# Kernel optimization log

Hardware: AMD Instinct MI355X
Metric: run time of the kernel (lower is better)

Reference implementation:

```python
import jax, jax.numpy as jnp
import numpy as np

MUL_S, MUL_V = 256, 128              # 256x0e + 128x1o hidden irreps
DIM_H = MUL_S + 3 * MUL_V            # 640
N_NODES = 100000
INV_SQRT3 = 3.0 ** -0.5
# e3nn 'element' path normalization: sqrt(ir_out.dim / sum_paths(mul1*mul2));
# for the 1o output the extra sqrt(3) cancels the 1/sqrt(3) of the wigner-3j,
# so every path ends up with the same constant.
C0 = (1.0 / (MUL_S + MUL_V)) ** 0.5


def _unif(key, shape, fan):
    # matches linear_layer_init: uniform(-a, a), a = sqrt(6/(mul1*mul2 + mul_out)), mul2 = 1
    a = (6.0 / fan) ** 0.5
    return jax.random.uniform(key, shape, minval=-a, maxval=a, dtype=jnp.float32)


def setup_inputs() -> dict:
    key = jax.random.key(0)
    ks = jax.random.split(key, 8)
    data_in = jax.random.normal(ks[0], (N_NODES, DIM_H + 4), dtype=jnp.float32)
    return {
        "data_in": data_in,
        "W_ss": _unif(ks[1], (MUL_S, MUL_S), MUL_S + MUL_S),      # 0e x 0e -> 0e (scalars)
        "W_vv": _unif(ks[2], (MUL_V, MUL_S), MUL_V + MUL_S),      # 1o x 1o -> 0e (scalars)
        "W_ss_g": _unif(ks[3], (MUL_S, MUL_V), MUL_S + MUL_V),    # 0e x 0e -> 0e (gates)
        "W_vv_g": _unif(ks[4], (MUL_V, MUL_V), MUL_V + MUL_V),    # 1o x 1o -> 0e (gates)
        "W_sv": _unif(ks[5], (MUL_S, MUL_V), MUL_S + MUL_V),      # 0e x 1o -> 1o
        "W_vs": _unif(ks[6], (MUL_V, MUL_V), MUL_V + MUL_V),      # 1o x 0e -> 1o
        "b": jnp.zeros((MUL_S,), dtype=jnp.float32),
    }


def reference(data_in, W_ss, W_vv, W_ss_g, W_vv_g, W_sv, W_vs, b):
    # split hidden / pos parts (forward does data_in[:, :-irreps_pos.dim] etc.)
    xs = data_in[:, :MUL_S]                           # [N, 256] 0e
    xv = data_in[:, MUL_S:DIM_H].reshape(-1, MUL_V, 3)  # [N, 128, 3] 1o
    ps = data_in[:, DIM_H:DIM_H + 1]                  # [N, 1] pos scalar
    pv = data_in[:, DIM_H + 1:]                       # [N, 3] pos vector

    # CG invariants feeding the 0e outputs
    s0 = xs * ps                                       # 0e x 0e path
    dot = jnp.einsum('nuk,nk->nu', xv, pv) * INV_SQRT3  # 1o x 1o -> 0e path, [N, 128]

    scal = C0 * (s0 @ W_ss + dot @ W_vv) + b           # [N, 256] scalars (+bias on N_trivial)
    gate = C0 * (s0 @ W_ss_g + dot @ W_vv_g)           # [N, 128] gates

    # 1o outputs: 0e x 1o and 1o x 0e paths
    v1 = (xs @ W_sv)[:, :, None] * pv[:, None, :]            # [N, 128, 3]
    v2 = jnp.einsum('nuk,uw->nwk', xv, W_vs) * ps[:, :, None]  # [N, 128, 3]
    vec = C0 * (v1 + v2)

    # Gate: Swish(beta=1) on scalars, sigmoid(gates) multiplying gated 1o irreps
    scal_out = scal * jax.nn.sigmoid(scal)
    vec_out = vec * jax.nn.sigmoid(gate)[:, :, None]
    return jnp.concatenate([scal_out, vec_out.reshape(-1, 3 * MUL_V)], axis=1)  # [N, 640]
```

## Files before the change

kernel.cpp:

```cpp
#include <hip/hip_runtime.h>
#include <hip/hip_bf16.h>

#define MUL_Sc 256
#define MUL_Vc 128
#define DIM_Hc 640
#define IN_COLS 644
#define KF 768
#define NT 32

#define C0F 0.05103103630798287f
#define INV_SQRT3F 0.57735026918962576f

typedef __attribute__((ext_vector_type(8))) short short8;
typedef __attribute__((ext_vector_type(4))) float f32x4;

#define MFMA(a, b, c) __builtin_amdgcn_mfma_f32_16x16x32_bf16((a), (b), (c), 0, 0, 0)

__device__ __forceinline__ unsigned short f2bf(float x) {
    union { float f; unsigned u; } v; v.f = x;
    unsigned r = v.u + 0x7fffu + ((v.u >> 16) & 1u);
    return (unsigned short)(r >> 16);
}
__device__ __forceinline__ float bf2f(unsigned short h) {
    union { unsigned u; float f; } v; v.u = ((unsigned)h) << 16;
    return v.f;
}

__global__ void prep_weights(const float* __restrict__ Wss, const float* __restrict__ Wvv,
                             const float* __restrict__ Wssg, const float* __restrict__ Wvvg,
                             const float* __restrict__ Wsv, const float* __restrict__ Wvs,
                             unsigned short* __restrict__ wt) {
    int i = blockIdx.x * 256 + threadIdx.x;
    const int N_SG = 384 * 384;
    const int N_SV = 128 * 256;
    const int N_VS = 128 * 128;
    if (i < N_SG) {
        int col = i / 384, k = i % 384;
        float v;
        if (col < 256) v = (k < 256) ? Wss[k * 256 + col] : Wvv[(k - 256) * 256 + col];
        else { int c = col - 256; v = (k < 256) ? Wssg[k * 128 + c] : Wvvg[(k - 256) * 128 + c]; }
        wt[i] = f2bf(v);
    } else if (i < N_SG + N_SV) {
        int j = i - N_SG; int col = j >> 8, k = j & 255;
        wt[i] = f2bf(Wsv[k * 128 + col]);
    } else if (i < N_SG + N_SV + N_VS) {
        int j = i - N_SG - N_SV; int col = j >> 7, k = j & 127;
        wt[i] = f2bf(Wvs[k * 128 + col]);
    }
}

__global__ __launch_bounds__(512, 4)
void fused_main(const float* __restrict__ din, const unsigned short* __restrict__ wt,
                const float* __restrict__ bias, float* __restrict__ out, int N) {
    __shared__ unsigned short feat[NT * KF];
    __shared__ float psv[NT * 4];

    const int tid = threadIdx.x;
    const int n0 = blockIdx.x * NT;

    {
        const int g = tid >> 4;
        const int j = tid & 15;
        int n = n0 + g; if (n >= N) n = N - 1;
        const float* row = din + (size_t)n * IN_COLS;
        float ps  = row[DIM_Hc];
        float pv0 = row[DIM_Hc + 1], pv1 = row[DIM_Hc + 2], pv2 = row[DIM_Hc + 3];
        if (j == 0) { psv[g*4+0] = ps; psv[g*4+1] = pv0; psv[g*4+2] = pv1; psv[g*4+3] = pv2; }
        char* fb = (char*)feat;
        const int swz  = (g & 7) << 4;
        const int rowb = g * (KF * 2);

        {
            int c = 16 * j;
            float4 x0 = *(const float4*)(row + c);
            float4 x1 = *(const float4*)(row + c + 4);
            float4 x2 = *(const float4*)(row + c + 8);
            float4 x3 = *(const float4*)(row + c + 12);
            short8 p0, p1;
            p0[0]=(short)f2bf(x0.x); p0[1]=(short)f2bf(x0.y); p0[2]=(short)f2bf(x0.z); p0[3]=(short)f2bf(x0.w);
            p0[4]=(short)f2bf(x1.x); p0[5]=(short)f2bf(x1.y); p0[6]=(short)f2bf(x1.z); p0[7]=(short)f2bf(x1.w);
            p1[0]=(short)f2bf(x2.x); p1[1]=(short)f2bf(x2.y); p1[2]=(short)f2bf(x2.z); p1[3]=(short)f2bf(x2.w);
            p1[4]=(short)f2bf(x3.x); p1[5]=(short)f2bf(x3.y); p1[6]=(short)f2bf(x3.z); p1[7]=(short)f2bf(x3.w);
            *(short8*)(fb + ((rowb + c * 2) ^ swz))       = p0;
            *(short8*)(fb + ((rowb + (c + 8) * 2) ^ swz)) = p1;
        }
        {
            int u0 = 8 * j;
            const float* p = row + MUL_Sc + 3 * u0;
            float e[24];
            #pragma unroll
            for (int q = 0; q < 6; ++q) {
                float4 v = *(const float4*)(p + 4 * q);
                e[4*q+0] = v.x; e[4*q+1] = v.y; e[4*q+2] = v.z; e[4*q+3] = v.w;
            }
            short8 dp, k0, k1, k2;
            #pragma unroll
            for (int m = 0; m < 8; ++m) {
                float a = e[3*m], b = e[3*m+1], c = e[3*m+2];
                dp[m] = (short)f2bf((a * pv0 + b * pv1 + c * pv2) * INV_SQRT3F);
                k0[m] = (short)f2bf(a);
                k1[m] = (short)f2bf(b);
                k2[m] = (short)f2bf(c);
            }
            *(short8*)(fb + ((rowb + (256 + u0) * 2) ^ swz)) = dp;
            *(short8*)(fb + ((rowb + (384 + u0) * 2) ^ swz)) = k0;
            *(short8*)(fb + ((rowb + (512 + u0) * 2) ^ swz)) = k1;
            *(short8*)(fb + ((rowb + (640 + u0) * 2) ^ swz)) = k2;
        }
    }
    __syncthreads();

    const int wave = tid >> 6;
    const int lane = tid & 63;
    const int l15  = lane & 15;
    const int lkb  = (lane >> 4) << 3;
    const char* fbr = (const char*)feat;
    const int swzr = (l15 & 7) << 4;

    const unsigned short* WTsg = wt;
    const unsigned short* WTsv = wt + 384 * 384;
    const unsigned short* WTvs = wt + 384 * 384 + 128 * 256;

    f32x4 acc1[3][2], acc2[3][2];
    #pragma unroll
    for (int t = 0; t < 3; ++t) {
        acc1[t][0] = (f32x4){0,0,0,0}; acc1[t][1] = (f32x4){0,0,0,0};
        acc2[t][0] = (f32x4){0,0,0,0}; acc2[t][1] = (f32x4){0,0,0,0};
    }
    const unsigned short* bp0 = WTsg + ((wave     ) * 16 + l15) * 384 + lkb;
    const unsigned short* bp1 = WTsg + ((wave +  8) * 16 + l15) * 384 + lkb;
    const unsigned short* bp2 = WTsg + ((wave + 16) * 16 + l15) * 384 + lkb;
    short8 b0a = *(const short8*)(bp0);      short8 b0b = *(const short8*)(bp0 + 32);
    short8 b1a = *(const short8*)(bp1);      short8 b1b = *(const short8*)(bp1 + 32);
    short8 b2a = *(const short8*)(bp2);      short8 b2b = *(const short8*)(bp2 + 32);
    #pragma unroll
    for (int ks = 0; ks < 12; ++ks) {
        int kf = ks * 32 + lkb;
        short8 a0 = *(const short8*)(fbr + ((l15 * 1536 + kf * 2) ^ swzr));
        short8 a1 = *(const short8*)(fbr + (((16 + l15) * 1536 + kf * 2) ^ swzr));
        short8 c0 = b0a, c1 = b1a, c2 = b2a;
        b0a = b0b; b1a = b1b; b2a = b2b;
        if (ks < 10) {
            b0b = *(const short8*)(bp0 + (ks + 2) * 32);
            b1b = *(const short8*)(bp1 + (ks + 2) * 32);
            b2b = *(const short8*)(bp2 + (ks + 2) * 32);
        }
        if (ks < 8) {
            acc1[0][0] = MFMA(a0, c0, acc1[0][0]); acc1[0][1] = MFMA(a1, c0, acc1[0][1]);
            acc1[1][0] = MFMA(a0, c1, acc1[1][0]); acc1[1][1] = MFMA(a1, c1, acc1[1][1]);
            acc1[2][0] = MFMA(a0, c2, acc1[2][0]); acc1[2][1] = MFMA(a1, c2, acc1[2][1]);
        } else {
            acc2[0][0] = MFMA(a0, c0, acc2[0][0]); acc2[0][1] = MFMA(a1, c0, acc2[0][1]);
            acc2[1][0] = MFMA(a0, c1, acc2[1][0]); acc2[1][1] = MFMA(a1, c1, acc2[1][1]);
            acc2[2][0] = MFMA(a0, c2, acc2[2][0]); acc2[2][1] = MFMA(a1, c2, acc2[2][1]);
        }
    }
    __syncthreads();

    f32x4 accA[2], accV[3][2];
    accA[0] = (f32x4){0,0,0,0}; accA[1] = (f32x4){0,0,0,0};
    #pragma unroll
    for (int k = 0; k < 3; ++k) { accV[k][0] = (f32x4){0,0,0,0}; accV[k][1] = (f32x4){0,0,0,0}; }

    const unsigned short* pA = WTsv + (wave * 16 + l15) * 256 + lkb;
    const unsigned short* pV = WTvs + (wave * 16 + l15) * 128 + lkb;
    short8 va = *(const short8*)(pA);      short8 vb = *(const short8*)(pA + 32);
    #pragma unroll
    for (int ks = 0; ks < 8; ++ks) {
        int kf = ks * 32 + lkb;
        short8 a0 = *(const short8*)(fbr + ((l15 * 1536 + kf * 2) ^ swzr));
        short8 a1 = *(const short8*)(fbr + (((16 + l15) * 1536 + kf * 2) ^ swzr));
        short8 cur = va; va = vb;
        if (ks < 6) vb = *(const short8*)(pA + (ks + 2) * 32);
        accA[0] = MFMA(a0, cur, accA[0]);
        accA[1] = MFMA(a1, cur, accA[1]);
    }
    short8 wa = *(const short8*)(pV);      short8 wb = *(const short8*)(pV + 32);
    #pragma unroll
    for (int ks = 0; ks < 4; ++ks) {
        short8 cur = wa; wa = wb;
        if (ks < 2) wb = *(const short8*)(pV + (ks + 2) * 32);
        #pragma unroll
        for (int k = 0; k < 3; ++k) {
            int kf = 384 + 128 * k + ks * 32 + lkb;
            short8 a0 = *(const short8*)(fbr + ((l15 * 1536 + kf * 2) ^ swzr));
            short8 a1 = *(const short8*)(fbr + (((16 + l15) * 1536 + kf * 2) ^ swzr));
            accV[k][0] = MFMA(a0, cur, accV[k][0]);
            accV[k][1] = MFMA(a1, cur, accV[k][1]);
        }
    }

    {
        const int rbase = (lane >> 4) << 2;
        float pss[2][4];
        #pragma unroll
        for (int s = 0; s < 2; ++s)
        #pragma unroll
        for (int i = 0; i < 4; ++i) pss[s][i] = psv[(s * 16 + rbase + i) * 4];

        #pragma unroll
        for (int t = 0; t < 2; ++t) {
            int col = (wave + t * 8) * 16 + l15;
            float bc = bias[col];
            #pragma unroll
            for (int s = 0; s < 2; ++s)
            #pragma unroll
            for (int i = 0; i < 4; ++i) {
                int nl = s * 16 + rbase + i;
                int n = n0 + nl;
                if (n < N) {
                    float sc = C0F * (pss[s][i] * acc1[t][s][i] + acc2[t][s][i]) + bc;
                    out[(size_t)n * DIM_Hc + col] = sc / (1.f + __expf(-sc));
                }
            }
        }
        char* fbw = (char*)feat;
        int gc = wave * 16 + l15;
        #pragma unroll
        for (int s = 0; s < 2; ++s)
        #pragma unroll
        for (int i = 0; i < 4; ++i) {
            int nl = s * 16 + rbase + i;
            float gt = C0F * (pss[s][i] * acc1[2][s][i] + acc2[2][s][i]);
            unsigned short sg = f2bf(1.f / (1.f + __expf(-gt)));
            *(unsigned short*)(fbw + ((nl * 1536 + (256 + gc) * 2) ^ ((nl & 7) << 4))) = sg;
        }
    }
    __syncthreads();

    {
        const int rbase = (lane >> 4) << 2;
        int u = wave * 16 + l15;
        #pragma unroll
        for (int s = 0; s < 2; ++s)
        #pragma unroll
        for (int i = 0; i < 4; ++i) {
            int nl = s * 16 + rbase + i;
            int n = n0 + nl;
            if (n >= N) continue;
            float sg  = bf2f(*(const unsigned short*)(fbr + ((nl * 1536 + (256 + u) * 2) ^ ((nl & 7) << 4))));
            float ps  = psv[nl * 4 + 0];
            float pv0 = psv[nl * 4 + 1], pv1 = psv[nl * 4 + 2], pv2 = psv[nl * 4 + 3];
            float av = accA[s][i];
            size_t ob = (size_t)n * DIM_Hc + MUL_Sc + 3 * u;
            out[ob + 0] = C0F * (av * pv0 + accV[0][s][i] * ps) * sg;
            out[ob + 1] = C0F * (av * pv1 + accV[1][s][i] * ps) * sg;
            out[ob + 2] = C0F * (av * pv2 + accV[2][s][i] * ps) * sg;
        }
    }
}

extern "C" void kernel_launch(void* const* d_in, const int* in_sizes, int n_in,
                              void* d_out, int out_size, void* d_ws, size_t ws_size,
                              hipStream_t stream) {
    const float* din  = (const float*)d_in[0];
    const float* Wss  = (const float*)d_in[1];
    const float* Wvv  = (const float*)d_in[2];
    const float* Wssg = (const float*)d_in[3];
    const float* Wvvg = (const float*)d_in[4];
    const float* Wsv  = (const float*)d_in[5];
    const float* Wvs  = (const float*)d_in[6];
    const float* bias = (const float*)d_in[7];
    float* out = (float*)d_out;
    unsigned short* wt = (unsigned short*)d_ws;

    const size_t WT_BYTES = (size_t)(384 * 384 + 128 * 256 + 128 * 128) * 2;
    if (ws_size < WT_BYTES) return;

    int N = in_sizes[0] / IN_COLS;

    int prep_total = 384 * 384 + 128 * 256 + 128 * 128;
    prep_weights<<<(prep_total + 255) / 256, 256, 0, stream>>>(Wss, Wvv, Wssg, Wvvg, Wsv, Wvs, wt);

    int nblocks = (N + NT - 1) / NT;
    fused_main<<<nblocks, 512, 0, stream>>>(din, wt, bias, out, N);
}
```

Baseline: 244.7 us.

## Stage weight tiles into LDS via double-buffered async global-to-LDS loads

Weight B-operands are no longer read per-wave straight from global memory. They are copied into a double-buffered, swizzled LDS tile with global_load_lds, and the copy of the next K-step overlaps the MFMAs on the current one. The gate sigmoid now stays in registers instead of round-tripping through LDS, and the two scalar accumulators are merged by scaling with ps mid-loop. The change adds about 96KB of LDS and many block-wide barriers, and lowers the occupancy hint from 4 to 2 blocks per CU.

Result: slower. 269.3 us (+10.0%).

```diff
diff --git a/kernel.cpp b/kernel.cpp
--- a/kernel.cpp
+++ b/kernel.cpp
@@ -2,7 +2,6 @@
 #include <hip/hip_bf16.h>
 
 #define MUL_Sc 256
-#define MUL_Vc 128
 #define DIM_Hc 640
 #define IN_COLS 644
 #define KF 768
@@ -21,9 +20,10 @@
     unsigned r = v.u + 0x7fffu + ((v.u >> 16) & 1u);
     return (unsigned short)(r >> 16);
 }
-__device__ __forceinline__ float bf2f(unsigned short h) {
-    union { unsigned u; float f; } v; v.u = ((unsigned)h) << 16;
-    return v.f;
+
+__device__ __forceinline__ void gload_lds16(const unsigned short* g, unsigned short* l) {
+    __builtin_amdgcn_global_load_lds((const __attribute__((address_space(1))) void*)g,
+                                     (__attribute__((address_space(3))) void*)l, 16, 0, 0);
 }
 
 __global__ void prep_weights(const float* __restrict__ Wss, const float* __restrict__ Wvv,
@@ -49,14 +49,34 @@
     }
 }
 
-__global__ __launch_bounds__(512, 4)
+__global__ __launch_bounds__(512, 2)
 void fused_main(const float* __restrict__ din, const unsigned short* __restrict__ wt,
                 const float* __restrict__ bias, float* __restrict__ out, int N) {
     __shared__ unsigned short feat[NT * KF];
+    __shared__ unsigned short ldsB[2][384 * 64];
     __shared__ float psv[NT * 4];
 
-    const int tid = threadIdx.x;
-    const int n0 = blockIdx.x * NT;
+    const int tid  = threadIdx.x;
+    const int wave = tid >> 6;
+    const int lane = tid & 63;
+    const int n0   = blockIdx.x * NT;
+
+    const unsigned short* WTsg = wt;
+    const unsigned short* WTsv = wt + 384 * 384;
+    const unsigned short* WTvs = wt + 384 * 384 + 128 * 256;
+
+    auto stage = [&](int buf, const unsigned short* W, int rs, int nr, int step) {
+        unsigned short* lb = &ldsB[buf][0] + wave * 512;
+        #pragma unroll
+        for (int m = 0; m < nr; ++m) {
+            int slot = m * 512 + tid;
+            int col  = slot >> 3;
+            int k8   = (slot & 7) ^ (col & 7);
+            gload_lds16(W + col * rs + step * 64 + k8 * 8, lb + m * 4096);
+        }
+    };
+
+    stage(0, WTsg, 384, 6, 0);
 
     {
         const int g = tid >> 4;
@@ -110,126 +130,121 @@
     }
     __syncthreads();
 
-    const int wave = tid >> 6;
-    const int lane = tid & 63;
-    const int l15  = lane & 15;
-    const int lkb  = (lane >> 4) << 3;
+    const int l15   = lane & 15;
+    const int lkb   = (lane >> 4) << 3;
+    const int chnk  = lane >> 4;
+    const int rbase = (lane >> 4) << 2;
     const char* fbr = (const char*)feat;
-    const int swzr = (l15 & 7) << 4;
-
-    const unsigned short* WTsg = wt;
-    const unsigned short* WTsv = wt + 384 * 384;
-    const unsigned short* WTvs = wt + 384 * 384 + 128 * 256;
-
-    f32x4 acc1[3][2], acc2[3][2];
-    #pragma unroll
-    for (int t = 0; t < 3; ++t) {
-        acc1[t][0] = (f32x4){0,0,0,0}; acc1[t][1] = (f32x4){0,0,0,0};
-        acc2[t][0] = (f32x4){0,0,0,0}; acc2[t][1] = (f32x4){0,0,0,0};
-    }
-    const unsigned short* bp0 = WTsg + ((wave     ) * 16 + l15) * 384 + lkb;
-    const unsigned short* bp1 = WTsg + ((wave +  8) * 16 + l15) * 384 + lkb;
-    const unsigned short* bp2 = WTsg + ((wave + 16) * 16 + l15) * 384 + lkb;
-    short8 b0a = *(const short8*)(bp0);      short8 b0b = *(const short8*)(bp0 + 32);
-    short8 b1a = *(const short8*)(bp1);      short8 b1b = *(const short8*)(bp1 + 32);
-    short8 b2a = *(const short8*)(bp2);      short8 b2b = *(const short8*)(bp2 + 32);
-    #pragma unroll
-    for (int ks = 0; ks < 12; ++ks) {
-        int kf = ks * 32 + lkb;
-        short8 a0 = *(const short8*)(fbr + ((l15 * 1536 + kf * 2) ^ swzr));
-        short8 a1 = *(const short8*)(fbr + (((16 + l15) * 1536 + kf * 2) ^ swzr));
-        short8 c0 = b0a, c1 = b1a, c2 = b2a;
-        b0a = b0b; b1a = b1b; b2a = b2b;
-        if (ks < 10) {
-            b0b = *(const short8*)(bp0 + (ks + 2) * 32);
-            b1b = *(const short8*)(bp1 + (ks + 2) * 32);
-            b2b = *(const short8*)(bp2 + (ks + 2) * 32);
-        }
-        if (ks < 8) {
-            acc1[0][0] = MFMA(a0, c0, acc1[0][0]); acc1[0][1] = MFMA(a1, c0, acc1[0][1]);
-            acc1[1][0] = MFMA(a0, c1, acc1[1][0]); acc1[1][1] = MFMA(a1, c1, acc1[1][1]);
-            acc1[2][0] = MFMA(a0, c2, acc1[2][0]); acc1[2][1] = MFMA(a1, c2, acc1[2][1]);
-        } else {
-            acc2[0][0] = MFMA(a0, c0, acc2[0][0]); acc2[0][1] = MFMA(a1, c0, acc2[0][1]);
-            acc2[1][0] = MFMA(a0, c1, acc2[1][0]); acc2[1][1] = MFMA(a1, c1, acc2[1][1]);
-            acc2[2][0] = MFMA(a0, c2, acc2[2][0]); acc2[2][1] = MFMA(a1, c2, acc2[2][1]);
-        }
-    }
-    __syncthreads();
-
-    f32x4 accA[2], accV[3][2];
+    const int swzr  = (l15 & 7) << 4;
+
+    float pss[2][4];
+    #pragma unroll
+    for (int s = 0; s < 2; ++s)
+    #pragma unroll
+    for (int i = 0; i < 4; ++i) pss[s][i] = psv[(s * 16 + rbase + i) * 4];
+
+    f32x4 accS[3][2];
+    #pragma unroll
+    for (int t = 0; t < 3; ++t) { accS[t][0] = (f32x4){0,0,0,0}; accS[t][1] = (f32x4){0,0,0,0}; }
+    f32x4 accA[2];
     accA[0] = (f32x4){0,0,0,0}; accA[1] = (f32x4){0,0,0,0};
+    f32x4 accV[3][2];
     #pragma unroll
     for (int k = 0; k < 3; ++k) { accV[k][0] = (f32x4){0,0,0,0}; accV[k][1] = (f32x4){0,0,0,0}; }
 
-    const unsigned short* pA = WTsv + (wave * 16 + l15) * 256 + lkb;
-    const unsigned short* pV = WTvs + (wave * 16 + l15) * 128 + lkb;
-    short8 va = *(const short8*)(pA);      short8 vb = *(const short8*)(pA + 32);
-    #pragma unroll
-    for (int ks = 0; ks < 8; ++ks) {
-        int kf = ks * 32 + lkb;
-        short8 a0 = *(const short8*)(fbr + ((l15 * 1536 + kf * 2) ^ swzr));
-        short8 a1 = *(const short8*)(fbr + (((16 + l15) * 1536 + kf * 2) ^ swzr));
-        short8 cur = va; va = vb;
-        if (ks < 6) vb = *(const short8*)(pA + (ks + 2) * 32);
-        accA[0] = MFMA(a0, cur, accA[0]);
-        accA[1] = MFMA(a1, cur, accA[1]);
-    }
-    short8 wa = *(const short8*)(pV);      short8 wb = *(const short8*)(pV + 32);
-    #pragma unroll
-    for (int ks = 0; ks < 4; ++ks) {
-        short8 cur = wa; wa = wb;
-        if (ks < 2) wb = *(const short8*)(pV + (ks + 2) * 32);
-        #pragma unroll
-        for (int k = 0; k < 3; ++k) {
-            int kf = 384 + 128 * k + ks * 32 + lkb;
+    auto sgstep = [&](int buf, int step) {
+        const char* B = (const char*)&ldsB[buf][0];
+        #pragma unroll
+        for (int ks = 0; ks < 2; ++ks) {
+            int kf = step * 64 + ks * 32 + lkb;
             short8 a0 = *(const short8*)(fbr + ((l15 * 1536 + kf * 2) ^ swzr));
             short8 a1 = *(const short8*)(fbr + (((16 + l15) * 1536 + kf * 2) ^ swzr));
-            accV[k][0] = MFMA(a0, cur, accV[k][0]);
-            accV[k][1] = MFMA(a1, cur, accV[k][1]);
-        }
-    }
+            int ch = ks * 4 + chnk;
+            #pragma unroll
+            for (int t = 0; t < 3; ++t) {
+                int col = (wave + t * 8) * 16 + l15;
+                short8 b = *(const short8*)(B + col * 128 + ((ch ^ (col & 7)) << 4));
+                accS[t][0] = MFMA(a0, b, accS[t][0]);
+                accS[t][1] = MFMA(a1, b, accS[t][1]);
+            }
+        }
+    };
+    auto svstep = [&](int buf, int step) {
+        const char* B = (const char*)&ldsB[buf][0];
+        #pragma unroll
+        for (int ks = 0; ks < 2; ++ks) {
+            int kf = step * 64 + ks * 32 + lkb;
+            short8 a0 = *(const short8*)(fbr + ((l15 * 1536 + kf * 2) ^ swzr));
+            short8 a1 = *(const short8*)(fbr + (((16 + l15) * 1536 + kf * 2) ^ swzr));
+            int ch = ks * 4 + chnk;
+            int col = wave * 16 + l15;
+            short8 b = *(const short8*)(B + col * 128 + ((ch ^ (col & 7)) << 4));
+            accA[0] = MFMA(a0, b, accA[0]);
+            accA[1] = MFMA(a1, b, accA[1]);
+        }
+    };
+    auto vsstep = [&](int buf, int step) {
+        const char* B = (const char*)&ldsB[buf][0];
+        #pragma unroll
+        for (int ks = 0; ks < 2; ++ks) {
+            int ch = ks * 4 + chnk;
+            int col = wave * 16 + l15;
+            short8 b = *(const short8*)(B + col * 128 + ((ch ^ (col & 7)) << 4));
+            #pragma unroll
+            for (int p = 0; p < 3; ++p) {
+                int kf = 384 + p * 128 + step * 64 + ks * 32 + lkb;
+                short8 a0 = *(const short8*)(fbr + ((l15 * 1536 + kf * 2) ^ swzr));
+                short8 a1 = *(const short8*)(fbr + (((16 + l15) * 1536 + kf * 2) ^ swzr));
+                accV[p][0] = MFMA(a0, b, accV[p][0]);
+                accV[p][1] = MFMA(a1, b, accV[p][1]);
+            }
+        }
+    };
+
+    stage(1, WTsg, 384, 6, 1);  sgstep(0, 0);  __syncthreads();
+    stage(0, WTsg, 384, 6, 2);  sgstep(1, 1);  __syncthreads();
+    stage(1, WTsg, 384, 6, 3);  sgstep(0, 2);  __syncthreads();
+    stage(0, WTsg, 384, 6, 4);  sgstep(1, 3);
+    #pragma unroll
+    for (int t = 0; t < 3; ++t)
+    #pragma unroll
+    for (int s = 0; s < 2; ++s)
+    #pragma unroll
+    for (int i = 0; i < 4; ++i) accS[t][s][i] *= pss[s][i];
+    __syncthreads();
+    stage(1, WTsg, 384, 6, 5);  sgstep(0, 4);  __syncthreads();
+    stage(0, WTsv, 256, 2, 0);  sgstep(1, 5);
+
+    #pragma unroll
+    for (int t = 0; t < 2; ++t) {
+        int col = (wave + t * 8) * 16 + l15;
+        float bc = bias[col];
+        #pragma unroll
+        for (int s = 0; s < 2; ++s)
+        #pragma unroll
+        for (int i = 0; i < 4; ++i) {
+            int n = n0 + s * 16 + rbase + i;
+            if (n < N) {
+                float sc = C0F * accS[t][s][i] + bc;
+                out[(size_t)n * DIM_Hc + col] = sc / (1.f + __expf(-sc));
+            }
+        }
+    }
+    float sgr[2][4];
+    #pragma unroll
+    for (int s = 0; s < 2; ++s)
+    #pragma unroll
+    for (int i = 0; i < 4; ++i) sgr[s][i] = 1.f / (1.f + __expf(-C0F * accS[2][s][i]));
+    __syncthreads();
+
+    stage(1, WTsv, 256, 2, 1);  svstep(0, 0);  __syncthreads();
+    stage(0, WTsv, 256, 2, 2);  svstep(1, 1);  __syncthreads();
+    stage(1, WTsv, 256, 2, 3);  svstep(0, 2);  __syncthreads();
+    stage(0, WTvs, 128, 2, 0);  svstep(1, 3);  __syncthreads();
+    stage(1, WTvs, 128, 2, 1);  vsstep(0, 0);  __syncthreads();
+                                vsstep(1, 1);
 
     {
-        const int rbase = (lane >> 4) << 2;
-        float pss[2][4];
-        #pragma unroll
-        for (int s = 0; s < 2; ++s)
-        #pragma unroll
-        for (int i = 0; i < 4; ++i) pss[s][i] = psv[(s * 16 + rbase + i) * 4];
-
-        #pragma unroll
-        for (int t = 0; t < 2; ++t) {
-            int col = (wave + t * 8) * 16 + l15;
-            float bc = bias[col];
-            #pragma unroll
-            for (int s = 0; s < 2; ++s)
-            #pragma unroll
-            for (int i = 0; i < 4; ++i) {
-                int nl = s * 16 + rbase + i;
-                int n = n0 + nl;
-                if (n < N) {
-                    float sc = C0F * (pss[s][i] * acc1[t][s][i] + acc2[t][s][i]) + bc;
-                    out[(size_t)n * DIM_Hc + col] = sc / (1.f + __expf(-sc));
-                }
-            }
-        }
-        char* fbw = (char*)feat;
-        int gc = wave * 16 + l15;
-        #pragma unroll
-        for (int s = 0; s < 2; ++s)
-        #pragma unroll
-        for (int i = 0; i < 4; ++i) {
-            int nl = s * 16 + rbase + i;
-            float gt = C0F * (pss[s][i] * acc1[2][s][i] + acc2[2][s][i]);
-            unsigned short sg = f2bf(1.f / (1.f + __expf(-gt)));
-            *(unsigned short*)(fbw + ((nl * 1536 + (256 + gc) * 2) ^ ((nl & 7) << 4))) = sg;
-        }
-    }
-    __syncthreads();
-
-    {
-        const int rbase = (lane >> 4) << 2;
         int u = wave * 16 + l15;
         #pragma unroll
         for (int s = 0; s < 2; ++s)
@@ -238,8 +253,8 @@
             int nl = s * 16 + rbase + i;
             int n = n0 + nl;
             if (n >= N) continue;
-            float sg  = bf2f(*(const unsigned short*)(fbr + ((nl * 1536 + (256 + u) * 2) ^ ((nl & 7) << 4))));
-            float ps  = psv[nl * 4 + 0];
+            float sg  = sgr[s][i];
+            float ps  = pss[s][i];
             float pv0 = psv[nl * 4 + 1], pv1 = psv[nl * 4 + 2], pv2 = psv[nl * 4 + 3];
             float av = accA[s][i];
             size_t ob = (size_t)n * DIM_Hc + MUL_Sc + 3 * u;
```

## Double node tile to 64 rows and keep gates in registers

Applied to the files above, without the earlier changes.

Raises the per-block node tile from 32 to 64 so each weight fragment loaded from global memory feeds four MFMA row tiles instead of two, halving weight traffic per node. The scalar/gate GEMM now uses a single accumulator per tile, scaled by ps between the two K segments, instead of separate accumulators. Gate sigmoids stay in registers rather than being written to shared memory and reread, which removes two block barriers. In exchange it doubles LDS use to about 96 KB, lowers the occupancy hint to 2 blocks per CU, raises register pressure, and drops the software prefetch of B fragments.

Result: faster. 234.5 us (-4.2%).

```diff
diff --git a/kernel.cpp b/kernel.cpp
--- a/kernel.cpp
+++ b/kernel.cpp
@@ -2,11 +2,10 @@
 #include <hip/hip_bf16.h>
 
 #define MUL_Sc 256
-#define MUL_Vc 128
 #define DIM_Hc 640
 #define IN_COLS 644
 #define KF 768
-#define NT 32
+#define NT 64
 
 #define C0F 0.05103103630798287f
 #define INV_SQRT3F 0.57735026918962576f
@@ -20,10 +19,6 @@
     union { float f; unsigned u; } v; v.f = x;
     unsigned r = v.u + 0x7fffu + ((v.u >> 16) & 1u);
     return (unsigned short)(r >> 16);
-}
-__device__ __forceinline__ float bf2f(unsigned short h) {
-    union { unsigned u; float f; } v; v.u = ((unsigned)h) << 16;
-    return v.f;
 }
 
 __global__ void prep_weights(const float* __restrict__ Wss, const float* __restrict__ Wvv,
@@ -49,7 +44,7 @@
     }
 }
 
-__global__ __launch_bounds__(512, 4)
+__global__ __launch_bounds__(512, 2)
 void fused_main(const float* __restrict__ din, const unsigned short* __restrict__ wt,
                 const float* __restrict__ bias, float* __restrict__ out, int N) {
     __shared__ unsigned short feat[NT * KF];
@@ -59,8 +54,8 @@
     const int n0 = blockIdx.x * NT;
 
     {
-        const int g = tid >> 4;
-        const int j = tid & 15;
+        const int g = tid >> 3;
+        const int j = tid & 7;
         int n = n0 + g; if (n >= N) n = N - 1;
         const float* row = din + (size_t)n * IN_COLS;
         float ps  = row[DIM_Hc];
@@ -70,8 +65,9 @@
         const int swz  = (g & 7) << 4;
         const int rowb = g * (KF * 2);
 
-        {
-            int c = 16 * j;
+        #pragma unroll
+        for (int half = 0; half < 2; ++half) {
+            int c = 32 * j + 16 * half;
             float4 x0 = *(const float4*)(row + c);
             float4 x1 = *(const float4*)(row + c + 4);
             float4 x2 = *(const float4*)(row + c + 8);
@@ -84,8 +80,9 @@
             *(short8*)(fb + ((rowb + c * 2) ^ swz))       = p0;
             *(short8*)(fb + ((rowb + (c + 8) * 2) ^ swz)) = p1;
         }
-        {
-            int u0 = 8 * j;
+        #pragma unroll
+        for (int half = 0; half < 2; ++half) {
+            int u0 = 16 * j + 8 * half;
             const float* p = row + MUL_Sc + 3 * u0;
             float e[24];
             #pragma unroll
@@ -114,6 +111,7 @@
     const int lane = tid & 63;
     const int l15  = lane & 15;
     const int lkb  = (lane >> 4) << 3;
+    const int rbase = (lane >> 4) << 2;
     const char* fbr = (const char*)feat;
     const int swzr = (l15 & 7) << 4;
 
@@ -121,131 +119,125 @@
     const unsigned short* WTsv = wt + 384 * 384;
     const unsigned short* WTvs = wt + 384 * 384 + 128 * 256;
 
-    f32x4 acc1[3][2], acc2[3][2];
-    #pragma unroll
-    for (int t = 0; t < 3; ++t) {
-        acc1[t][0] = (f32x4){0,0,0,0}; acc1[t][1] = (f32x4){0,0,0,0};
-        acc2[t][0] = (f32x4){0,0,0,0}; acc2[t][1] = (f32x4){0,0,0,0};
-    }
-    const unsigned short* bp0 = WTsg + ((wave     ) * 16 + l15) * 384 + lkb;
-    const unsigned short* bp1 = WTsg + ((wave +  8) * 16 + l15) * 384 + lkb;
-    const unsigned short* bp2 = WTsg + ((wave + 16) * 16 + l15) * 384 + lkb;
-    short8 b0a = *(const short8*)(bp0);      short8 b0b = *(const short8*)(bp0 + 32);
-    short8 b1a = *(const short8*)(bp1);      short8 b1b = *(const short8*)(bp1 + 32);
-    short8 b2a = *(const short8*)(bp2);      short8 b2b = *(const short8*)(bp2 + 32);
-    #pragma unroll
-    for (int ks = 0; ks < 12; ++ks) {
-        int kf = ks * 32 + lkb;
-        short8 a0 = *(const short8*)(fbr + ((l15 * 1536 + kf * 2) ^ swzr));
-        short8 a1 = *(const short8*)(fbr + (((16 + l15) * 1536 + kf * 2) ^ swzr));
-        short8 c0 = b0a, c1 = b1a, c2 = b2a;
-        b0a = b0b; b1a = b1b; b2a = b2b;
-        if (ks < 10) {
-            b0b = *(const short8*)(bp0 + (ks + 2) * 32);
-            b1b = *(const short8*)(bp1 + (ks + 2) * 32);
-            b2b = *(const short8*)(bp2 + (ks + 2) * 32);
-        }
-        if (ks < 8) {
-            acc1[0][0] = MFMA(a0, c0, acc1[0][0]); acc1[0][1] = MFMA(a1, c0, acc1[0][1]);
-            acc1[1][0] = MFMA(a0, c1, acc1[1][0]); acc1[1][1] = MFMA(a1, c1, acc1[1][1]);
-            acc1[2][0] = MFMA(a0, c2, acc1[2][0]); acc1[2][1] = MFMA(a1, c2, acc1[2][1]);
-        } else {
-            acc2[0][0] = MFMA(a0, c0, acc2[0][0]); acc2[0][1] = MFMA(a1, c0, acc2[0][1]);
-            acc2[1][0] = MFMA(a0, c1, acc2[1][0]); acc2[1][1] = MFMA(a1, c1, acc2[1][1]);
-            acc2[2][0] = MFMA(a0, c2, acc2[2][0]); acc2[2][1] = MFMA(a1, c2, acc2[2][1]);
-        }
-    }
-    __syncthreads();
-
-    f32x4 accA[2], accV[3][2];
-    accA[0] = (f32x4){0,0,0,0}; accA[1] = (f32x4){0,0,0,0};
-    #pragma unroll
-    for (int k = 0; k < 3; ++k) { accV[k][0] = (f32x4){0,0,0,0}; accV[k][1] = (f32x4){0,0,0,0}; }
-
-    const unsigned short* pA = WTsv + (wave * 16 + l15) * 256 + lkb;
-    const unsigned short* pV = WTvs + (wave * 16 + l15) * 128 + lkb;
-    short8 va = *(const short8*)(pA);      short8 vb = *(const short8*)(pA + 32);
+    float pss[4][4];
+    #pragma unroll
+    for (int m = 0; m < 4; ++m)
+    #pragma unroll
+    for (int i = 0; i < 4; ++i) pss[m][i] = psv[(m * 16 + rbase + i) * 4];
+
+    f32x4 accS[3][4];
+    #pragma unroll
+    for (int t = 0; t < 3; ++t)
+    #pragma unroll
+    for (int m = 0; m < 4; ++m) accS[t][m] = (f32x4){0,0,0,0};
+
     #pragma unroll
     for (int ks = 0; ks < 8; ++ks) {
         int kf = ks * 32 + lkb;
-        short8 a0 = *(const short8*)(fbr + ((l15 * 1536 + kf * 2) ^ swzr));
-        short8 a1 = *(const short8*)(fbr + (((16 + l15) * 1536 + kf * 2) ^ swzr));
-        short8 cur = va; va = vb;
-        if (ks < 6) vb = *(const short8*)(pA + (ks + 2) * 32);
-        accA[0] = MFMA(a0, cur, accA[0]);
-        accA[1] = MFMA(a1, cur, accA[1]);
-    }
-    short8 wa = *(const short8*)(pV);      short8 wb = *(const short8*)(pV + 32);
+        short8 a[4];
+        #pragma unroll
+        for (int m = 0; m < 4; ++m)
+            a[m] = *(const short8*)(fbr + (((m * 16 + l15) * 1536 + kf * 2) ^ swzr));
+        #pragma unroll
+        for (int t = 0; t < 3; ++t) {
+            int ct = wave + t * 8;
+            short8 b = *(const short8*)(WTsg + (ct * 16 + l15) * 384 + ks * 32 + lkb);
+            #pragma unroll
+            for (int m = 0; m < 4; ++m) accS[t][m] = MFMA(a[m], b, accS[t][m]);
+        }
+    }
+    #pragma unroll
+    for (int t = 0; t < 3; ++t)
+    #pragma unroll
+    for (int m = 0; m < 4; ++m)
+    #pragma unroll
+    for (int i = 0; i < 4; ++i) accS[t][m][i] *= pss[m][i];
     #pragma unroll
     for (int ks = 0; ks < 4; ++ks) {
-        short8 cur = wa; wa = wb;
-        if (ks < 2) wb = *(const short8*)(pV + (ks + 2) * 32);
-        #pragma unroll
-        for (int k = 0; k < 3; ++k) {
-            int kf = 384 + 128 * k + ks * 32 + lkb;
-            short8 a0 = *(const short8*)(fbr + ((l15 * 1536 + kf * 2) ^ swzr));
-            short8 a1 = *(const short8*)(fbr + (((16 + l15) * 1536 + kf * 2) ^ swzr));
-            accV[k][0] = MFMA(a0, cur, accV[k][0]);
-            accV[k][1] = MFMA(a1, cur, accV[k][1]);
+        int kf = 256 + ks * 32 + lkb;
+        short8 a[4];
+        #pragma unroll
+        for (int m = 0; m < 4; ++m)
+            a[m] = *(const short8*)(fbr + (((m * 16 + l15) * 1536 + kf * 2) ^ swzr));
+        #pragma unroll
+        for (int t = 0; t < 3; ++t) {
+            int ct = wave + t * 8;
+            short8 b = *(const short8*)(WTsg + (ct * 16 + l15) * 384 + 256 + ks * 32 + lkb);
+            #pragma unroll
+            for (int m = 0; m < 4; ++m) accS[t][m] = MFMA(a[m], b, accS[t][m]);
+        }
+    }
+
+    #pragma unroll
+    for (int t = 0; t < 2; ++t) {
+        int col = (wave + t * 8) * 16 + l15;
+        float bc = bias[col];
+        #pragma unroll
+        for (int m = 0; m < 4; ++m)
+        #pragma unroll
+        for (int i = 0; i < 4; ++i) {
+            int n = n0 + m * 16 + rbase + i;
+            if (n < N) {
+                float sc = C0F * accS[t][m][i] + bc;
+                out[(size_t)n * DIM_Hc + col] = sc / (1.f + __expf(-sc));
+            }
+        }
+    }
+    float sgr[4][4];
+    #pragma unroll
+    for (int m = 0; m < 4; ++m)
+    #pragma unroll
+    for (int i = 0; i < 4; ++i) sgr[m][i] = 1.f / (1.f + __expf(-C0F * accS[2][m][i]));
+
+    f32x4 accA[4], accV[3][4];
+    #pragma unroll
+    for (int m = 0; m < 4; ++m) accA[m] = (f32x4){0,0,0,0};
+    #pragma unroll
+    for (int k = 0; k < 3; ++k)
+    #pragma unroll
+    for (int m = 0; m < 4; ++m) accV[k][m] = (f32x4){0,0,0,0};
+
+    #pragma unroll
+    for (int ks = 0; ks < 8; ++ks) {
+        int kf = ks * 32 + lkb;
+        short8 b = *(const short8*)(WTsv + (wave * 16 + l15) * 256 + ks * 32 + lkb);
+        #pragma unroll
+        for (int m = 0; m < 4; ++m) {
+            short8 a = *(const short8*)(fbr + (((m * 16 + l15) * 1536 + kf * 2) ^ swzr));
+            accA[m] = MFMA(a, b, accA[m]);
+        }
+    }
+    #pragma unroll
+    for (int ks = 0; ks < 4; ++ks) {
+        short8 b = *(const short8*)(WTvs + (wave * 16 + l15) * 128 + ks * 32 + lkb);
+        #pragma unroll
+        for (int p = 0; p < 3; ++p) {
+            int kf = 384 + 128 * p + ks * 32 + lkb;
+            #pragma unroll
+            for (int m = 0; m < 4; ++m) {
+                short8 a = *(const short8*)(fbr + (((m * 16 + l15) * 1536 + kf * 2) ^ swzr));
+                accV[p][m] = MFMA(a, b, accV[p][m]);
+            }
         }
     }
 
     {
-        const int rbase = (lane >> 4) << 2;
-        float pss[2][4];
-        #pragma unroll
-        for (int s = 0; s < 2; ++s)
-        #pragma unroll
-        for (int i = 0; i < 4; ++i) pss[s][i] = psv[(s * 16 + rbase + i) * 4];
-
-        #pragma unroll
-        for (int t = 0; t < 2; ++t) {
-            int col = (wave + t * 8) * 16 + l15;
-            float bc = bias[col];
-            #pragma unroll
-            for (int s = 0; s < 2; ++s)
-            #pragma unroll
-            for (int i = 0; i < 4; ++i) {
-                int nl = s * 16 + rbase + i;
-                int n = n0 + nl;
-                if (n < N) {
-                    float sc = C0F * (pss[s][i] * acc1[t][s][i] + acc2[t][s][i]) + bc;
-                    out[(size_t)n * DIM_Hc + col] = sc / (1.f + __expf(-sc));
-                }
-            }
-        }
-        char* fbw = (char*)feat;
-        int gc = wave * 16 + l15;
-        #pragma unroll
-        for (int s = 0; s < 2; ++s)
+        int u = wave * 16 + l15;
+        #pragma unroll
+        for (int m = 0; m < 4; ++m)
         #pragma unroll
         for (int i = 0; i < 4; ++i) {
-            int nl = s * 16 + rbase + i;
-            float gt = C0F * (pss[s][i] * acc1[2][s][i] + acc2[2][s][i]);
-            unsigned short sg = f2bf(1.f / (1.f + __expf(-gt)));
-            *(unsigned short*)(fbw + ((nl * 1536 + (256 + gc) * 2) ^ ((nl & 7) << 4))) = sg;
-        }
-    }
-    __syncthreads();
-
-    {
-        const int rbase = (lane >> 4) << 2;
-        int u = wave * 16 + l15;
-        #pragma unroll
-        for (int s = 0; s < 2; ++s)
-        #pragma unroll
-        for (int i = 0; i < 4; ++i) {
-            int nl = s * 16 + rbase + i;
+            int nl = m * 16 + rbase + i;
             int n = n0 + nl;
             if (n >= N) continue;
-            float sg  = bf2f(*(const unsigned short*)(fbr + ((nl * 1536 + (256 + u) * 2) ^ ((nl & 7) << 4))));
-            float ps  = psv[nl * 4 + 0];
+            float sg  = sgr[m][i];
+            float ps  = pss[m][i];
             float pv0 = psv[nl * 4 + 1], pv1 = psv[nl * 4 + 2], pv2 = psv[nl * 4 + 3];
-            float av = accA[s][i];
+            float av = accA[m][i];
             size_t ob = (size_t)n * DIM_Hc + MUL_Sc + 3 * u;
-            out[ob + 0] = C0F * (av * pv0 + accV[0][s][i] * ps) * sg;
-            out[ob + 1] = C0F * (av * pv1 + accV[1][s][i] * ps) * sg;
-            out[ob + 2] = C0F * (av * pv2 + accV[2][s][i] * ps) * sg;
+            out[ob + 0] = C0F * (av * pv0 + accV[0][m][i] * ps) * sg;
+            out[ob + 1] = C0F * (av * pv1 + accV[1][m][i] * ps) * sg;
+            out[ob + 2] = C0F * (av * pv2 + accV[2][m][i] * ps) * sg;
         }
     }
 }
```
